# Kernel optimization log

Hardware: AMD Instinct MI355X
Metric: run time of the kernel (lower is better)

The kernel has to match this reference:

```python
import jax, jax.numpy as jnp
import numpy as np
import math

# Model dims
B, S, D, H = 2, 2048, 1024, 16
DH = D // H  # 64
TAU = 0.2
EPS = 1e-5

# Unit-scaling scale factors (constraint = gmean of fwd/bwd scales)
# Linear: gmean(fan_in**-0.5, fan_out**-0.5) = (fan_in*fan_out)**-0.25
# Matmul (m,k)@(k,n): gmean(k**-0.5, n**-0.5, m**-0.5) = (m*k*n)**(-1/6)
# Softmax over dim n: gmean(n/1.31, n/1.65) (empirical constants from unit_scaling)
# GELU: gmean(1/0.588, 1/0.675)
MM_SCALE = (S * S * DH) ** (-1.0 / 6.0)
SM_SCALE = S / math.sqrt(1.31 * 1.65)
GELU_SCALE = (0.588 * 0.675) ** -0.5
SQRT_TAU = math.sqrt(TAU)
SQRT_1MTAU = math.sqrt(1.0 - TAU)


def u_linear(x, w, b=None):
    fan_out, fan_in = w.shape
    scale = (fan_in * fan_out) ** -0.25
    y = x @ w.T
    if b is not None:
        y = y + b
    return y * scale


def layer_norm(x, w, b):
    m = jnp.mean(x, axis=-1, keepdims=True)
    v = jnp.mean(jnp.square(x - m), axis=-1, keepdims=True)
    return (x - m) * jax.lax.rsqrt(v + EPS) * w + b


def setup_inputs() -> dict:
    key = jax.random.key(0)
    ks = jax.random.split(key, 8)
    return {
        "x": jax.random.normal(ks[0], (B, S, D), jnp.float32),
        "w_qkv": jax.random.normal(ks[1], (3 * D, D), jnp.float32),
        "w_o": jax.random.normal(ks[2], (D, D), jnp.float32),
        "w1": jax.random.normal(ks[3], (4 * D, D), jnp.float32),
        "b1": jnp.zeros((4 * D,), jnp.float32),
        "w2": jax.random.normal(ks[4], (D, 4 * D), jnp.float32),
        "b2": jnp.zeros((D,), jnp.float32),
        "ln1_w": jnp.ones((D,), jnp.float32),
        "ln1_b": jnp.zeros((D,), jnp.float32),
        "ln2_w": jnp.ones((D,), jnp.float32),
        "ln2_b": jnp.zeros((D,), jnp.float32),
    }


def reference(x, w_qkv, w_o, w1, b1, w2, b2, ln1_w, ln1_b, ln2_w, ln2_b):
    # --- MHSA branch (residual_split forward is identity; tau enters at add) ---
    skip = x
    h = layer_norm(x, ln1_w, ln1_b)
    qkv = u_linear(h, w_qkv)  # [B,S,3D]
    # einops 'b s (d z h) -> z b h s d' with z=3, h=H
    qkv = qkv.reshape(B, S, DH, 3, H)
    q = jnp.transpose(qkv[:, :, :, 0, :], (0, 3, 1, 2))  # [B,H,S,DH]
    k = jnp.transpose(qkv[:, :, :, 1, :], (0, 3, 1, 2))
    v = jnp.transpose(qkv[:, :, :, 2, :], (0, 3, 1, 2))
    scores = jnp.einsum("bhsd,bhtd->bhst", q, k) * MM_SCALE
    attn = jax.nn.softmax(scores, axis=-1) * SM_SCALE
    # dropout: eval mode -> identity
    av = jnp.einsum("bhst,bhtd->bhsd", attn, v) * MM_SCALE
    av = jnp.transpose(av, (0, 2, 1, 3)).reshape(B, S, D)  # b h s d -> b s (h d)
    attn_out = u_linear(av, w_o)
    x = SQRT_TAU * attn_out + SQRT_1MTAU * skip  # residual_add

    # --- MLP branch ---
    skip = x
    h = layer_norm(x, ln2_w, ln2_b)
    h = u_linear(h, w1, b1)
    h = jax.nn.gelu(h, approximate=False) * GELU_SCALE
    h = u_linear(h, w2, b2)
    return SQRT_TAU * h + SQRT_1MTAU * skip
```

## Files before the change

kernel.cpp:

```cpp
#include <hip/hip_runtime.h>
#include <hip/hip_bf16.h>
#include <math.h>

typedef __hip_bfloat16 bf16;
typedef __attribute__((ext_vector_type(8))) short short8;
typedef __attribute__((ext_vector_type(4))) float floatx4;

#define B_   2
#define S_   2048
#define D_   1024
#define H_   16
#define DH_  64
#define BS_  4096
#define D3_  3072
#define DF_  4096

__device__ __forceinline__ float tof(float v) { return v; }
__device__ __forceinline__ float tof(bf16 v) { return __bfloat162float(v); }

__device__ __forceinline__ void gload_lds16(const bf16* g, bf16* l) {
  __builtin_amdgcn_global_load_lds(
      (const __attribute__((address_space(1))) unsigned int*)g,
      (__attribute__((address_space(3))) unsigned int*)l, 16, 0, 0);
}

#define VMCNT(n) asm volatile("s_waitcnt vmcnt(" #n ")" ::: "memory")

__global__ __launch_bounds__(256) void cvt_all(
    const float* __restrict__ wqkv, const float* __restrict__ wo,
    const float* __restrict__ w1, bf16* __restrict__ wqb,
    bf16* __restrict__ wob, bf16* __restrict__ w1b) {
  const int g = blockIdx.x * 256 + threadIdx.x;
  if (g < 786432) {
    const int n2 = g >> 8;
    const int col = (g & 255) * 4;
    const int z = n2 >> 10, hh = (n2 >> 6) & 15, d = n2 & 63;
    const int n = d * 48 + z * 16 + hh;
    float4 v = *(const float4*)(wqkv + (size_t)n * 1024 + col);
    bf16 o[4] = {__float2bfloat16(v.x), __float2bfloat16(v.y),
                 __float2bfloat16(v.z), __float2bfloat16(v.w)};
    *(unsigned long long*)(wqb + (size_t)n2 * 1024 + col) =
        *(unsigned long long*)o;
  } else if (g < 1048576) {
    const int g2 = g - 786432;
    float4 v = ((const float4*)wo)[g2];
    bf16 o[4] = {__float2bfloat16(v.x), __float2bfloat16(v.y),
                 __float2bfloat16(v.z), __float2bfloat16(v.w)};
    ((unsigned long long*)wob)[g2] = *(unsigned long long*)o;
  } else {
    const int g2 = g - 1048576;
    float4 v = ((const float4*)w1)[g2];
    bf16 o[4] = {__float2bfloat16(v.x), __float2bfloat16(v.y),
                 __float2bfloat16(v.z), __float2bfloat16(v.w)};
    ((unsigned long long*)w1b)[g2] = *(unsigned long long*)o;
  }
}

template <bool FUSE, bool INIT, typename TA, typename TS>
__global__ __launch_bounds__(256) void resid_ln_kernel(
    const TA* __restrict__ a, const TA* __restrict__ a2,
    const TS* __restrict__ skip,
    const float* __restrict__ w, const float* __restrict__ bias,
    bf16* __restrict__ hout, float st, float s1t,
    float* __restrict__ oinit, const float* __restrict__ b2,
    float cb, float cs) {
  const int row = blockIdx.x;
  const int tid = threadIdx.x;
  const int base = tid * 4;
  const size_t roff = (size_t)row * D_;

  float xv[4];
#pragma unroll
  for (int i = 0; i < 4; i++) {
    float v = tof(a[roff + base + i]);
    if (FUSE) v = st * (v + tof(a2[roff + base + i]))
                  + s1t * tof(skip[roff + base + i]);
    xv[i] = v;
  }
  if (INIT) {
#pragma unroll
    for (int i = 0; i < 4; i++)
      oinit[roff + base + i] = cs * xv[i] + cb * b2[base + i];
  }

  float ls = 0.f, lq = 0.f;
#pragma unroll
  for (int i = 0; i < 4; i++) { ls += xv[i]; lq += xv[i] * xv[i]; }

  __shared__ float ssum[256];
  __shared__ float ssq[256];
  ssum[tid] = ls; ssq[tid] = lq;
  __syncthreads();
  for (int off = 128; off > 0; off >>= 1) {
    if (tid < off) { ssum[tid] += ssum[tid + off]; ssq[tid] += ssq[tid + off]; }
    __syncthreads();
  }
  const float mean = ssum[0] * (1.0f / D_);
  const float var  = ssq[0] * (1.0f / D_) - mean * mean;
  const float rstd = rsqrtf(var + 1e-5f);

#pragma unroll
  for (int i = 0; i < 4; i++) {
    float v = (xv[i] - mean) * rstd * w[base + i] + bias[base + i];
    hout[roff + base + i] = __float2bfloat16(v);
  }
}

__global__ __launch_bounds__(256) void reduce_ffn2(
    const bf16* __restrict__ p0, const bf16* __restrict__ p1,
    float* __restrict__ out, float sc) {
  const size_t i = ((size_t)blockIdx.x * 256 + threadIdx.x) * 8;
  short8 a = *(const short8*)(p0 + i);
  short8 b = *(const short8*)(p1 + i);
  bf16 t0[8], t1[8];
  *(short8*)t0 = a; *(short8*)t1 = b;
  float4 o0 = *(float4*)(out + i);
  float4 o1 = *(float4*)(out + i + 4);
#pragma unroll
  for (int e = 0; e < 4; e++) {
    ((float*)&o0)[e] += sc * (__bfloat162float(t0[e]) + __bfloat162float(t1[e]));
    ((float*)&o1)[e] += sc * (__bfloat162float(t0[e + 4]) + __bfloat162float(t1[e + 4]));
  }
  *(float4*)(out + i) = o0;
  *(float4*)(out + i + 4) = o1;
}

__global__ __launch_bounds__(256) void combine_attn(
    const bf16* __restrict__ O0, const bf16* __restrict__ O1,
    const float* __restrict__ l0, const float* __restrict__ l1,
    bf16* __restrict__ att, float sc) {
  const size_t i = ((size_t)blockIdx.x * 256 + threadIdx.x) * 8;
  const int srow = (int)(i >> 10);
  const int h = (int)(i >> 6) & 15;
  const float inv = sc / (l0[srow * H_ + h] + l1[srow * H_ + h]);
  short8 a = *(const short8*)(O0 + i);
  short8 b = *(const short8*)(O1 + i);
  bf16 t0[8], t1[8], o[8];
  *(short8*)t0 = a; *(short8*)t1 = b;
#pragma unroll
  for (int e = 0; e < 8; e++)
    o[e] = __float2bfloat16((tof(t0[e]) + tof(t1[e])) * inv);
  *(short8*)(att + i) = *(short8*)o;
}

template <int EPI, bool FCVT, typename TC>
__global__ __launch_bounds__(512, 2) void gemm_mfma256(
    const bf16* __restrict__ A, const bf16* __restrict__ Bw,
    TC* __restrict__ C, TC* __restrict__ Chi,
    int M, int N, int K, float scale,
    const float* __restrict__ bias, float st,
    const float* __restrict__ cvsrc, bf16* __restrict__ cvdst, int cvn4) {
  const int nbx = N >> 8;
  const int nwg = nbx * (M >> 8);
  if (FCVT && (int)blockIdx.x >= nwg) {
    const int nth = ((int)gridDim.x - nwg) * 512;
    for (int i = ((int)blockIdx.x - nwg) * 512 + (int)threadIdx.x; i < cvn4;
         i += nth) {
      float4 v = ((const float4*)cvsrc)[i];
      bf16 o[4] = {__float2bfloat16(v.x), __float2bfloat16(v.y),
                   __float2bfloat16(v.z), __float2bfloat16(v.w)};
      ((unsigned long long*)cvdst)[i] = *(unsigned long long*)o;
    }
    return;
  }

  __shared__ __align__(16) bf16 As[2][2][128][64];
  __shared__ __align__(16) bf16 Bs[2][2][128][64];

  const int tid = threadIdx.x;
  const int lane = tid & 63;
  const int w = tid >> 6;
  const int wm = w >> 2;
  const int wn = w & 3;
  const int quad = lane >> 4;
  const int l16 = lane & 15;

  int bid = blockIdx.x;
  bid = (bid & 7) * (nwg >> 3) + (bid >> 3);
  const size_t bm = (size_t)(bid / nbx) * 256;
  const size_t bn = (size_t)(bid % nbx) * 256;

  const bf16* gsrc[4][2];
  bf16* ldsp[4][2];
#pragma unroll
  for (int i = 0; i < 2; i++) {
    const int G = tid + i * 512;
    const int cr = G >> 3;
    const int gs8 = ((G & 7) ^ (cr & 7)) * 8;
    const int ra = ((cr >> 6) << 7) + (cr & 63);
    const int rb = ((cr >> 5) << 6) + (cr & 31);
    gsrc[0][i] = A  + (bm + ra) * (size_t)K + gs8;
    gsrc[2][i] = A  + (bm + ra + 64) * (size_t)K + gs8;
    gsrc[1][i] = Bw + (bn + rb) * (size_t)K + gs8;
    gsrc[3][i] = Bw + (bn + rb + 32) * (size_t)K + gs8;
    ldsp[0][i] = &As[0][0][0][0] + G * 8;
    ldsp[2][i] = &As[0][1][0][0] + G * 8;
    ldsp[1][i] = &Bs[0][0][0][0] + G * 8;
    ldsp[3][i] = &Bs[0][1][0][0] + G * 8;
  }

  auto STAGE = [&](int c, int tn) {
    const int boff = (tn & 1) * 16384;
    gload_lds16(gsrc[c][0] + (size_t)tn * 64, ldsp[c][0] + boff);
    gload_lds16(gsrc[c][1] + (size_t)tn * 64, ldsp[c][1] + boff);
  };

  const int ksw0 = (quad ^ (l16 & 7)) * 8;
  const int ksw1 = ((4 + quad) ^ (l16 & 7)) * 8;

  floatx4 acc[8][4];
#pragma unroll
  for (int i = 0; i < 8; i++)
#pragma unroll
    for (int j = 0; j < 4; j++) acc[i][j] = {0.f, 0.f, 0.f, 0.f};

  short8 af[4][2], bv[2][2];

  auto READ_A = [&](int b, int h) {
#pragma unroll
    for (int mf = 0; mf < 4; mf++) {
      const bf16* p = &As[b][h][wm * 64 + mf * 16 + l16][0];
      af[mf][0] = *(const short8*)(p + ksw0);
      af[mf][1] = *(const short8*)(p + ksw1);
    }
  };
  auto READ_B = [&](int b, int bh) {
#pragma unroll
    for (int nf = 0; nf < 2; nf++) {
      const bf16* p = &Bs[b][bh][wn * 32 + nf * 16 + l16][0];
      bv[nf][0] = *(const short8*)(p + ksw0);
      bv[nf][1] = *(const short8*)(p + ksw1);
    }
  };
  auto MFMA16 = [&](int mb, int nb) {
#pragma unroll
    for (int mf = 0; mf < 4; mf++)
#pragma unroll
      for (int nf = 0; nf < 2; nf++) {
        floatx4 c = acc[mb + mf][nb + nf];
        c = __builtin_amdgcn_mfma_f32_16x16x32_bf16(af[mf][0], bv[nf][0], c, 0, 0, 0);
        c = __builtin_amdgcn_mfma_f32_16x16x32_bf16(af[mf][1], bv[nf][1], c, 0, 0, 0);
        acc[mb + mf][nb + nf] = c;
      }
  };

  STAGE(0, 0); STAGE(1, 0); STAGE(2, 0); STAGE(3, 0);
  VMCNT(4);
  __builtin_amdgcn_s_barrier();
  __builtin_amdgcn_sched_barrier(0);

  const int NT = K >> 6;
#pragma unroll 1
  for (int t = 0; t < NT; t++) {
    const int b = t & 1;
    const bool nl = (t + 1 < NT);
    READ_A(b, 0);
    READ_B(b, 0);
    if (nl) STAGE(0, t + 1);
    __builtin_amdgcn_s_barrier();
    __builtin_amdgcn_sched_barrier(0);
    __builtin_amdgcn_s_setprio(1);
    MFMA16(0, 0);
    __builtin_amdgcn_s_setprio(0);
    if (nl) { VMCNT(2); } else { VMCNT(0); }
    __builtin_amdgcn_s_barrier();
    __builtin_amdgcn_sched_barrier(0);
    READ_B(b, 1);
    if (nl) STAGE(1, t + 1);
    __builtin_amdgcn_s_barrier();
    __builtin_amdgcn_sched_barrier(0);
    __builtin_amdgcn_s_setprio(1);
    MFMA16(0, 2);
    __builtin_amdgcn_s_setprio(0);
    __builtin_amdgcn_s_barrier();
    __builtin_amdgcn_sched_barrier(0);
    READ_A(b, 1);
    if (nl) STAGE(2, t + 1);
    __builtin_amdgcn_s_barrier();
    __builtin_amdgcn_sched_barrier(0);
    __builtin_amdgcn_s_setprio(1);
    MFMA16(4, 2);
    __builtin_amdgcn_s_setprio(0);
    __builtin_amdgcn_s_barrier();
    __builtin_amdgcn_sched_barrier(0);
    READ_B(b, 0);
    if (nl) STAGE(3, t + 1);
    __builtin_amdgcn_s_barrier();
    __builtin_amdgcn_sched_barrier(0);
    __builtin_amdgcn_s_setprio(1);
    MFMA16(4, 0);
    __builtin_amdgcn_s_setprio(0);
    if (nl) { VMCNT(4); } else { VMCNT(0); }
    __builtin_amdgcn_s_barrier();
    __builtin_amdgcn_sched_barrier(0);
  }

  TC* Cb = (bm < 1024) ? C : Chi;
  const size_t rsub = (bm < 1024) ? 0 : 1024;
  float sc_eff = scale;
  if (EPI == 2) sc_eff = (bn < 1024) ? st : scale;
  float bias4[4];
  if (EPI == 1) {
#pragma unroll
    for (int j = 0; j < 4; j++) bias4[j] = bias[bn + wn * 64 + j * 16 + l16];
  }
#pragma unroll
  for (int mi = 0; mi < 8; mi++) {
    const size_t r0 =
        bm - rsub + wm * 128 + (mi >> 2) * 64 + (mi & 3) * 16 + quad * 4;
#pragma unroll
    for (int r = 0; r < 4; r++) {
      const size_t rowoff = (r0 + r) * (size_t)N + bn + wn * 64 + l16;
#pragma unroll
      for (int j = 0; j < 4; j++) {
        float v = acc[mi][j][r];
        if (EPI == 2) {
          Cb[rowoff + j * 16] = __float2bfloat16(v * sc_eff);
        } else {
          float u = (v + bias4[j]) * scale;
          float tt = u * (0.7978845608f + 0.0356774081f * u * u);
          float e = __builtin_amdgcn_exp2f(tt * 2.8853900818f);
          float th = 1.0f - 2.0f * __builtin_amdgcn_rcpf(e + 1.0f);
          Cb[rowoff + j * 16] =
              __float2bfloat16(0.5f * u * (1.0f + th) * st);
        }
      }
    }
  }
}

__global__ __launch_bounds__(512, 2) void gemm_mfma128(
    const bf16* __restrict__ A, const bf16* __restrict__ Ahi,
    const bf16* __restrict__ Bw,
    bf16* __restrict__ C, bf16* __restrict__ C2, int M, int N, int K) {
  __shared__ __align__(16) bf16 As[2][2][128][64];
  __shared__ __align__(16) bf16 Bs[2][2][64][64];

  const int tid = threadIdx.x;
  const int lane = tid & 63;
  const int w = tid >> 6;
  const int wm = w >> 2;
  const int wn = w & 3;
  const int quad = lane >> 4;
  const int l16 = lane & 15;

  const int nbx = N >> 7;
  const int nwg = nbx * (M >> 8) * 2;
  int bid = blockIdx.x;
  bid = (bid & 7) * (nwg >> 3) + (bid >> 3);
  const int split = bid & 1;
  const int tile = bid >> 1;
  const size_t bm = (size_t)(tile / nbx) * 256;
  const size_t bn = (size_t)(tile % nbx) * 128;
  const int lda = K * 2;
  const int koff = split * K;

  const bf16* Ab = (bm < 1024) ? A : Ahi;
  const size_t bmr = (bm < 1024) ? bm : bm - 1024;

  const bf16* gA[2][2];
  bf16* lA[2][2];
#pragma unroll
  for (int i = 0; i < 2; i++) {
    const int G = tid + i * 512;
    const int cr = G >> 3;
    const int gs8 = ((G & 7) ^ (cr & 7)) * 8;
    const int ra = ((cr >> 6) << 7) + (cr & 63);
    gA[0][i] = Ab + (bmr + ra) * (size_t)lda + koff + gs8;
    gA[1][i] = Ab + (bmr + ra + 64) * (size_t)lda + koff + gs8;
    lA[0][i] = &As[0][0][0][0] + G * 8;
    lA[1][i] = &As[0][1][0][0] + G * 8;
  }
  const bf16* gB[2];
  bf16* lB[2];
  {
    const int cr = tid >> 3;
    const int gs8 = ((tid & 7) ^ (cr & 7)) * 8;
    gB[0] = Bw + (bn + cr) * (size_t)lda + koff + gs8;
    gB[1] = Bw + (bn + 64 + cr) * (size_t)lda + koff + gs8;
    lB[0] = &Bs[0][0][0][0] + tid * 8;
    lB[1] = &Bs[0][1][0][0] + tid * 8;
  }

  auto STAGE_A = [&](int h, int tn) {
    const int boff = (tn & 1) * 16384;
    gload_lds16(gA[h][0] + (size_t)tn * 64, lA[h][0] + boff);
    gload_lds16(gA[h][1] + (size_t)tn * 64, lA[h][1] + boff);
  };
  auto STAGE_B = [&](int bh, int tn) {
    const int boff = (tn & 1) * 8192;
    gload_lds16(gB[bh] + (size_t)tn * 64, lB[bh] + boff);
  };

  const int ksw0 = (quad ^ (l16 & 7)) * 8;
  const int ksw1 = ((4 + quad) ^ (l16 & 7)) * 8;

  floatx4 acc[8][2];
#pragma unroll
  for (int i = 0; i < 8; i++)
#pragma unroll
    for (int j = 0; j < 2; j++) acc[i][j] = {0.f, 0.f, 0.f, 0.f};

  short8 af[4][2], bv[2][2];

  auto READ_A = [&](int b, int h) {
#pragma unroll
    for (int mf = 0; mf < 4; mf++) {
      const bf16* p = &As[b][h][wm * 64 + mf * 16 + l16][0];
      af[mf][0] = *(const short8*)(p + ksw0);
      af[mf][1] = *(const short8*)(p + ksw1);
    }
  };
  auto READ_BNF = [&](int b, int nf) {
    const bf16* p = &Bs[b][wn >> 1][(wn & 1) * 32 + nf * 16 + l16][0];
    bv[nf][0] = *(const short8*)(p + ksw0);
    bv[nf][1] = *(const short8*)(p + ksw1);
  };
  auto MFMA8 = [&](int mb, int nf) {
#pragma unroll
    for (int mf = 0; mf < 4; mf++) {
      floatx4 c = acc[mb + mf][nf];
      c = __builtin_amdgcn_mfma_f32_16x16x32_bf16(af[mf][0], bv[nf][0], c, 0, 0, 0);
      c = __builtin_amdgcn_mfma_f32_16x16x32_bf16(af[mf][1], bv[nf][1], c, 0, 0, 0);
      acc[mb + mf][nf] = c;
    }
  };

  STAGE_A(0, 0); STAGE_B(0, 0); STAGE_B(1, 0); STAGE_A(1, 0);
  VMCNT(2);
  __builtin_amdgcn_s_barrier();
  __builtin_amdgcn_sched_barrier(0);

  const int NT = K >> 6;
#pragma unroll 1
  for (int t = 0; t < NT; t++) {
    const int b = t & 1;
    const bool nl = (t + 1 < NT);
    READ_A(b, 0);
    READ_BNF(b, 0);
    if (nl) STAGE_A(0, t + 1);
    __builtin_amdgcn_s_barrier();
    __builtin_amdgcn_sched_barrier(0);
    __builtin_amdgcn_s_setprio(1);
    MFMA8(0, 0);
    __builtin_amdgcn_s_setprio(0);
    __builtin_amdgcn_s_barrier();
    __builtin_amdgcn_sched_barrier(0);
    READ_BNF(b, 1);
    if (nl) STAGE_B(0, t + 1);
    __builtin_amdgcn_s_barrier();
    __builtin_amdgcn_sched_barrier(0);
    __builtin_amdgcn_s_setprio(1);
    MFMA8(0, 1);
    __builtin_amdgcn_s_setprio(0);
    if (nl) { VMCNT(3); } else { VMCNT(0); }
    __builtin_amdgcn_s_barrier();
    __builtin_amdgcn_sched_barrier(0);
    READ_A(b, 1);
    if (nl) STAGE_B(1, t + 1);
    __builtin_amdgcn_s_barrier();
    __builtin_amdgcn_sched_barrier(0);
    __builtin_amdgcn_s_setprio(1);
    MFMA8(4, 1);
    __builtin_amdgcn_s_setprio(0);
    __builtin_amdgcn_s_barrier();
    __builtin_amdgcn_sched_barrier(0);
    if (nl) STAGE_A(1, t + 1);
    __builtin_amdgcn_s_barrier();
    __builtin_amdgcn_sched_barrier(0);
    __builtin_amdgcn_s_setprio(1);
    MFMA8(4, 0);
    __builtin_amdgcn_s_setprio(0);
    if (nl) { VMCNT(2); } else { VMCNT(0); }
    __builtin_amdgcn_s_barrier();
    __builtin_amdgcn_sched_barrier(0);
  }

  bf16* dst = split ? C2 : C;
#pragma unroll
  for (int mi = 0; mi < 8; mi++) {
    const size_t r0 = bm + wm * 128 + (mi >> 2) * 64 + (mi & 3) * 16 + quad * 4;
#pragma unroll
    for (int r = 0; r < 4; r++) {
      const size_t rowoff = (r0 + r) * (size_t)N + bn + wn * 32 + l16;
#pragma unroll
      for (int j = 0; j < 2; j++)
        dst[rowoff + j * 16] = __float2bfloat16(acc[mi][j][r]);
    }
  }
}

__global__ __launch_bounds__(512) void flash_attn_mfma(
    const bf16* __restrict__ qkv, bf16* __restrict__ O0,
    bf16* __restrict__ O1, float* __restrict__ lb0,
    float* __restrict__ lb1) {
  const int flat = (blockIdx.z * H_ + blockIdx.y) * 32 + blockIdx.x;
  const int g8 = flat & 7, slot = flat >> 3;
  const int hf = g8 * 4 + (slot >> 5);
  const int rem = slot & 31;
  const int qb = (rem >> 1) * 128;
  const int half = rem & 1;
  const int h = hf & 15, b = hf >> 4;

  const int tid = threadIdx.x;
  const int lane = tid & 63;
  const int wv = tid >> 6;
  const int quad = lane >> 4;
  const int l16 = lane & 15;

  __shared__ __align__(16) bf16 Ks[2][64][64];
  __shared__ __align__(16) bf16 Vt[2][64][64];
  __shared__ __align__(16) bf16 Ps[128][64];

  const bf16* Qb_ = qkv + (size_t)b * S_ * D3_ + h * DH_;
  const bf16* Kb_ = Qb_ + 1024 + (size_t)half * 1024 * D3_;
  const bf16* Vb_ = Qb_ + 2048 + (size_t)half * 1024 * D3_;

  short8 bq0, bq1;
  {
    const bf16* qrow = Qb_ + (size_t)(qb + wv * 16 + l16) * D3_ + quad * 8;
    bq0 = *(const short8*)(qrow);
    bq1 = *(const short8*)(qrow + 32);
  }

  float l_part = 0.f;
  floatx4 o[4];
#pragma unroll
  for (int fd = 0; fd < 4; fd++) o[fd] = {0.f, 0.f, 0.f, 0.f};

  const int prow = wv * 16 + l16;
  const int psw = (prow & 7) << 4;
  char* pbase = (char*)&Ps[0][0] + prow * 128;

  const bf16* ksrc =
      Kb_ + (size_t)(tid >> 3) * D3_ + (((tid & 7) ^ ((tid >> 3) & 7)) * 8);
  bf16* kdst = &Ks[0][0][0] + tid * 8;
  const int vj = tid & 63, vd = (tid >> 6) * 8;
  const int vjg = vj >> 3, vjr = vj & 7;

  const int ksw0 = (quad ^ (l16 & 7)) * 8;
  const int ksw1 = ((4 + quad) ^ (l16 & 7)) * 8;

  gload_lds16(ksrc, kdst);
  uint4 vreg = *(const uint4*)(Vb_ + (size_t)vj * D3_ + vd);

  const int NT = 1024 / 64;
#pragma unroll 1
  for (int t = 0; t < NT; t++) {
    const int cur = t & 1;
    {
      bf16 tmp[8];
      *(uint4*)tmp = vreg;
#pragma unroll
      for (int e = 0; e < 8; e++)
        Vt[cur][vd + e][((vjg ^ e) << 3) | vjr] = tmp[e];
    }
    __syncthreads();

    if (t + 1 < NT) {
      gload_lds16(ksrc + (size_t)(t + 1) * 64 * D3_, kdst + (cur ^ 1) * 4096);
      vreg = *(const uint4*)(Vb_ + (size_t)((t + 1) * 64 + vj) * D3_ + vd);
    }

    float st[4][4];
    __builtin_amdgcn_s_setprio(1);
#pragma unroll
    for (int fk = 0; fk < 4; fk++) {
      const bf16* kp = &Ks[cur][fk * 16 + l16][0];
      short8 ak0 = *(const short8*)(kp + ksw0);
      short8 ak1 = *(const short8*)(kp + ksw1);
      floatx4 acc = {0.f, 0.f, 0.f, 0.f};
      acc = __builtin_amdgcn_mfma_f32_16x16x32_bf16(ak0, bq0, acc, 0, 0, 0);
      acc = __builtin_amdgcn_mfma_f32_16x16x32_bf16(ak1, bq1, acc, 0, 0, 0);
#pragma unroll
      for (int r = 0; r < 4; r++) st[fk][r] = acc[r];
    }
    __builtin_amdgcn_s_setprio(0);

#pragma unroll
    for (int fk = 0; fk < 2; fk++) {
      bf16 pk[4];
#pragma unroll
      for (int r = 0; r < 4; r++) {
        const float p = __builtin_amdgcn_exp2f(st[fk][r]);
        l_part += p;
        pk[r] = __float2bfloat16(p);
      }
      *(uint2*)(pbase + ((fk * 32 + quad * 8) ^ psw)) = *(uint2*)pk;
    }
    short8 ap0 = *(const short8*)(pbase + ((quad * 16) ^ psw));
#pragma unroll
    for (int fk = 2; fk < 4; fk++) {
      bf16 pk[4];
#pragma unroll
      for (int r = 0; r < 4; r++) {
        const float p = __builtin_amdgcn_exp2f(st[fk][r]);
        l_part += p;
        pk[r] = __float2bfloat16(p);
      }
      *(uint2*)(pbase + ((fk * 32 + quad * 8) ^ psw)) = *(uint2*)pk;
    }
    short8 ap1 = *(const short8*)(pbase + ((64 + quad * 16) ^ psw));

    __builtin_amdgcn_s_setprio(1);
#pragma unroll
    for (int fd = 0; fd < 4; fd++) {
      const bf16* vp = &Vt[cur][fd * 16 + l16][0];
      short8 bv0 = *(const short8*)(vp + ksw0);
      short8 bv1 = *(const short8*)(vp + ksw1);
      o[fd] = __builtin_amdgcn_mfma_f32_16x16x32_bf16(ap0, bv0, o[fd], 0, 0, 0);
      o[fd] = __builtin_amdgcn_mfma_f32_16x16x32_bf16(ap1, bv1, o[fd], 0, 0, 0);
    }
    __builtin_amdgcn_s_setprio(0);
  }

  l_part += __shfl_xor(l_part, 16);
  l_part += __shfl_xor(l_part, 32);

  bf16* Oo = half ? O1 : O0;
  float* lo = half ? lb1 : lb0;
  if (quad == 0)
    lo[(size_t)(b * S_ + qb + wv * 16 + l16) * H_ + h] = l_part;
#pragma unroll
  for (int r = 0; r < 4; r++) {
    const size_t base =
        ((size_t)(b * S_ + qb + wv * 16 + quad * 4 + r)) * D_ + h * DH_;
#pragma unroll
    for (int fd = 0; fd < 4; fd++)
      Oo[base + fd * 16 + l16] = __float2bfloat16(o[fd][r]);
  }
}

extern "C" void kernel_launch(void* const* d_in, const int* in_sizes, int n_in,
                              void* d_out, int out_size, void* d_ws, size_t ws_size,
                              hipStream_t stream) {
  const float* x     = (const float*)d_in[0];
  const float* w_qkv = (const float*)d_in[1];
  const float* w_o   = (const float*)d_in[2];
  const float* w1    = (const float*)d_in[3];
  const float* b1    = (const float*)d_in[4];
  const float* w2    = (const float*)d_in[5];
  const float* b2    = (const float*)d_in[6];
  const float* ln1w  = (const float*)d_in[7];
  const float* ln1b  = (const float*)d_in[8];
  const float* ln2w  = (const float*)d_in[9];
  const float* ln2b  = (const float*)d_in[10];
  float* out = (float*)d_out;
  bf16* ws  = (bf16*)d_ws;

  bf16* h1   = ws;
  bf16* wqb  = ws + 4194304;
  bf16* wob  = ws + 7340032;
  bf16* qkv  = ws + 8388608;
  bf16* w2b  = ws + 20971520;
  bf16* w1b  = ws + 25165824;
  bf16* Ob0  = (bf16*)out;
  bf16* Ob1  = (bf16*)out + 4194304;
  float* l0f = (float*)(ws + 4194304);
  float* l1f = l0f + 65536;
  bf16* att  = ws;
  bf16* Po   = ws + 8388608;
  bf16* h2   = ws + 4194304;
  bf16* gl   = ws;
  bf16* gh   = ws + 8388608;
  bf16* Pf0  = ws + 4194304;
  bf16* Pf1  = ws + 25165824;

  const float MM_SCALE   = (float)pow((double)S_ * S_ * DH_, -1.0 / 6.0);
  const float SM_SCALE   = (float)((double)S_ / sqrt(1.31 * 1.65));
  const float GELU_SCALE = (float)pow(0.588 * 0.675, -0.5);
  const float SQRT_TAU   = (float)sqrt(0.2);
  const float SQRT_1MT   = (float)sqrt(0.8);
  const float LOG2E      = 1.4426950408889634f;
  const float qkv_scale  = (float)pow((double)D_ * D3_, -0.25);
  const float o_scale    = (float)pow((double)D_ * D_, -0.25);
  const float w1_scale   = (float)pow((double)D_ * DF_, -0.25);
  const float w2_scale   = (float)pow((double)DF_ * D_, -0.25);

  cvt_all<<<8192, 256, 0, stream>>>(w_qkv, w_o, w1, wqb, wob, w1b);
  resid_ln_kernel<false, false, float, float><<<BS_, 256, 0, stream>>>(
      x, nullptr, nullptr, ln1w, ln1b, h1, 0.f, 0.f, nullptr, nullptr, 0.f, 0.f);
  gemm_mfma256<2, true, bf16><<<dim3(256), 512, 0, stream>>>(
      h1, wqb, qkv, qkv + (size_t)1024 * D3_, BS_, D3_, D_, qkv_scale,
      nullptr, qkv_scale * MM_SCALE * LOG2E, w2, w2b, D_ * DF_ / 4);
  flash_attn_mfma<<<dim3(32, H_, B_), 512, 0, stream>>>(
      qkv, Ob0, Ob1, l0f, l1f);
  combine_attn<<<2048, 256, 0, stream>>>(
      Ob0, Ob1, l0f, l1f, att, SM_SCALE * MM_SCALE);
  gemm_mfma128<<<dim3(256), 512, 0, stream>>>(
      att, att + (size_t)1024 * D_, wob, Po, Po + (size_t)BS_ * D_,
      BS_, D_, D_ / 2);
  resid_ln_kernel<true, true, bf16, float><<<BS_, 256, 0, stream>>>(
      Po, Po + (size_t)BS_ * D_, x, ln2w, ln2b, h2,
      SQRT_TAU * o_scale, SQRT_1MT, out, b2, SQRT_TAU * w2_scale, SQRT_1MT);
  gemm_mfma256<1, false, bf16><<<dim3(256), 512, 0, stream>>>(
      h2, w1b, gl, gh, BS_, DF_, D_, w1_scale, b1, GELU_SCALE,
      nullptr, nullptr, 0);
  gemm_mfma128<<<dim3(256), 512, 0, stream>>>(
      gl, gh, w2b, Pf0, Pf1, BS_, D_, DF_ / 2);
  reduce_ffn2<<<2048, 256, 0, stream>>>(Pf0, Pf1, out, SQRT_TAU * w2_scale);
}
```

Measured before the change: 332.3 us.

## Double query rows per attention block and fuse LN1 into weight convert

The flash attention kernel now processes two 128-row query groups per block, so each loaded K/V tile is reused for 256 queries and the grid is halved. The first layer norm is folded into the weight conversion kernel as extra blocks, removing a separate launch. This trades higher register and LDS use per block, and fewer blocks in flight, for less K/V load traffic. The fused layer norm computes variance in one pass as E[x^2]-mean^2.

```diff
diff --git a/kernel.cpp b/kernel.cpp
--- a/kernel.cpp
+++ b/kernel.cpp
@@ -29,8 +29,40 @@
 __global__ __launch_bounds__(256) void cvt_all(
     const float* __restrict__ wqkv, const float* __restrict__ wo,
     const float* __restrict__ w1, bf16* __restrict__ wqb,
-    bf16* __restrict__ wob, bf16* __restrict__ w1b) {
-  const int g = blockIdx.x * 256 + threadIdx.x;
+    bf16* __restrict__ wob, bf16* __restrict__ w1b,
+    const float* __restrict__ x, const float* __restrict__ ln1w,
+    const float* __restrict__ ln1b, bf16* __restrict__ h1) {
+  __shared__ float ssum[256];
+  __shared__ float ssq[256];
+  const int bid = blockIdx.x;
+  const int tid = threadIdx.x;
+  if (bid >= 8192) {
+    const int row = bid - 8192;
+    const int base = tid * 4;
+    const size_t roff = (size_t)row * D_;
+    float xv[4];
+#pragma unroll
+    for (int i = 0; i < 4; i++) xv[i] = x[roff + base + i];
+    float ls = 0.f, lq = 0.f;
+#pragma unroll
+    for (int i = 0; i < 4; i++) { ls += xv[i]; lq += xv[i] * xv[i]; }
+    ssum[tid] = ls; ssq[tid] = lq;
+    __syncthreads();
+    for (int off = 128; off > 0; off >>= 1) {
+      if (tid < off) { ssum[tid] += ssum[tid + off]; ssq[tid] += ssq[tid + off]; }
+      __syncthreads();
+    }
+    const float mean = ssum[0] * (1.0f / D_);
+    const float var  = ssq[0] * (1.0f / D_) - mean * mean;
+    const float rstd = rsqrtf(var + 1e-5f);
+#pragma unroll
+    for (int i = 0; i < 4; i++) {
+      float v = (xv[i] - mean) * rstd * ln1w[base + i] + ln1b[base + i];
+      h1[roff + base + i] = __float2bfloat16(v);
+    }
+    return;
+  }
+  const int g = bid * 256 + tid;
   if (g < 786432) {
     const int n2 = g >> 8;
     const int col = (g & 255) * 4;
@@ -494,11 +526,11 @@
     const bf16* __restrict__ qkv, bf16* __restrict__ O0,
     bf16* __restrict__ O1, float* __restrict__ lb0,
     float* __restrict__ lb1) {
-  const int flat = (blockIdx.z * H_ + blockIdx.y) * 32 + blockIdx.x;
+  const int flat = (blockIdx.z * H_ + blockIdx.y) * 16 + blockIdx.x;
   const int g8 = flat & 7, slot = flat >> 3;
-  const int hf = g8 * 4 + (slot >> 5);
-  const int rem = slot & 31;
-  const int qb = (rem >> 1) * 128;
+  const int hf = g8 * 4 + (slot >> 4);
+  const int rem = slot & 15;
+  const int qb = (rem >> 1) * 256;
   const int half = rem & 1;
   const int h = hf & 15, b = hf >> 4;
 
@@ -510,27 +542,33 @@
 
   __shared__ __align__(16) bf16 Ks[2][64][64];
   __shared__ __align__(16) bf16 Vt[2][64][64];
-  __shared__ __align__(16) bf16 Ps[128][64];
+  __shared__ __align__(16) bf16 Ps[256][64];
 
   const bf16* Qb_ = qkv + (size_t)b * S_ * D3_ + h * DH_;
   const bf16* Kb_ = Qb_ + 1024 + (size_t)half * 1024 * D3_;
   const bf16* Vb_ = Qb_ + 2048 + (size_t)half * 1024 * D3_;
 
-  short8 bq0, bq1;
-  {
-    const bf16* qrow = Qb_ + (size_t)(qb + wv * 16 + l16) * D3_ + quad * 8;
-    bq0 = *(const short8*)(qrow);
-    bq1 = *(const short8*)(qrow + 32);
-  }
-
-  float l_part = 0.f;
-  floatx4 o[4];
-#pragma unroll
-  for (int fd = 0; fd < 4; fd++) o[fd] = {0.f, 0.f, 0.f, 0.f};
+  short8 bq[2][2];
+#pragma unroll
+  for (int qg = 0; qg < 2; qg++) {
+    const bf16* qrow =
+        Qb_ + (size_t)(qb + qg * 128 + wv * 16 + l16) * D3_ + quad * 8;
+    bq[qg][0] = *(const short8*)(qrow);
+    bq[qg][1] = *(const short8*)(qrow + 32);
+  }
+
+  float l_part[2] = {0.f, 0.f};
+  floatx4 o[2][4];
+#pragma unroll
+  for (int qg = 0; qg < 2; qg++)
+#pragma unroll
+    for (int fd = 0; fd < 4; fd++) o[qg][fd] = {0.f, 0.f, 0.f, 0.f};
 
   const int prow = wv * 16 + l16;
   const int psw = (prow & 7) << 4;
-  char* pbase = (char*)&Ps[0][0] + prow * 128;
+  char* pb[2];
+  pb[0] = (char*)&Ps[0][0] + prow * 128;
+  pb[1] = pb[0] + 128 * 128;
 
   const bf16* ksrc =
       Kb_ + (size_t)(tid >> 3) * D3_ + (((tid & 7) ^ ((tid >> 3) & 7)) * 8);
@@ -562,45 +600,44 @@
       vreg = *(const uint4*)(Vb_ + (size_t)((t + 1) * 64 + vj) * D3_ + vd);
     }
 
-    float st[4][4];
+    float st[2][4][4];
     __builtin_amdgcn_s_setprio(1);
 #pragma unroll
     for (int fk = 0; fk < 4; fk++) {
       const bf16* kp = &Ks[cur][fk * 16 + l16][0];
       short8 ak0 = *(const short8*)(kp + ksw0);
       short8 ak1 = *(const short8*)(kp + ksw1);
-      floatx4 acc = {0.f, 0.f, 0.f, 0.f};
-      acc = __builtin_amdgcn_mfma_f32_16x16x32_bf16(ak0, bq0, acc, 0, 0, 0);
-      acc = __builtin_amdgcn_mfma_f32_16x16x32_bf16(ak1, bq1, acc, 0, 0, 0);
-#pragma unroll
-      for (int r = 0; r < 4; r++) st[fk][r] = acc[r];
-    }
-    __builtin_amdgcn_s_setprio(0);
-
-#pragma unroll
-    for (int fk = 0; fk < 2; fk++) {
-      bf16 pk[4];
-#pragma unroll
-      for (int r = 0; r < 4; r++) {
-        const float p = __builtin_amdgcn_exp2f(st[fk][r]);
-        l_part += p;
-        pk[r] = __float2bfloat16(p);
+#pragma unroll
+      for (int qg = 0; qg < 2; qg++) {
+        floatx4 acc = {0.f, 0.f, 0.f, 0.f};
+        acc = __builtin_amdgcn_mfma_f32_16x16x32_bf16(ak0, bq[qg][0], acc, 0, 0, 0);
+        acc = __builtin_amdgcn_mfma_f32_16x16x32_bf16(ak1, bq[qg][1], acc, 0, 0, 0);
+#pragma unroll
+        for (int r = 0; r < 4; r++) st[qg][fk][r] = acc[r];
       }
-      *(uint2*)(pbase + ((fk * 32 + quad * 8) ^ psw)) = *(uint2*)pk;
-    }
-    short8 ap0 = *(const short8*)(pbase + ((quad * 16) ^ psw));
-#pragma unroll
-    for (int fk = 2; fk < 4; fk++) {
-      bf16 pk[4];
-#pragma unroll
-      for (int r = 0; r < 4; r++) {
-        const float p = __builtin_amdgcn_exp2f(st[fk][r]);
-        l_part += p;
-        pk[r] = __float2bfloat16(p);
+    }
+    __builtin_amdgcn_s_setprio(0);
+
+#pragma unroll
+    for (int qg = 0; qg < 2; qg++)
+#pragma unroll
+      for (int fk = 0; fk < 4; fk++) {
+        bf16 pk[4];
+#pragma unroll
+        for (int r = 0; r < 4; r++) {
+          const float p = __builtin_amdgcn_exp2f(st[qg][fk][r]);
+          l_part[qg] += p;
+          pk[r] = __float2bfloat16(p);
+        }
+        *(uint2*)(pb[qg] + ((fk * 32 + quad * 8) ^ psw)) = *(uint2*)pk;
       }
-      *(uint2*)(pbase + ((fk * 32 + quad * 8) ^ psw)) = *(uint2*)pk;
-    }
-    short8 ap1 = *(const short8*)(pbase + ((64 + quad * 16) ^ psw));
+
+    short8 ap[2][2];
+#pragma unroll
+    for (int qg = 0; qg < 2; qg++) {
+      ap[qg][0] = *(const short8*)(pb[qg] + ((quad * 16) ^ psw));
+      ap[qg][1] = *(const short8*)(pb[qg] + ((64 + quad * 16) ^ psw));
+    }
 
     __builtin_amdgcn_s_setprio(1);
 #pragma unroll
@@ -608,26 +645,33 @@
       const bf16* vp = &Vt[cur][fd * 16 + l16][0];
       short8 bv0 = *(const short8*)(vp + ksw0);
       short8 bv1 = *(const short8*)(vp + ksw1);
-      o[fd] = __builtin_amdgcn_mfma_f32_16x16x32_bf16(ap0, bv0, o[fd], 0, 0, 0);
-      o[fd] = __builtin_amdgcn_mfma_f32_16x16x32_bf16(ap1, bv1, o[fd], 0, 0, 0);
-    }
-    __builtin_amdgcn_s_setprio(0);
-  }
-
-  l_part += __shfl_xor(l_part, 16);
-  l_part += __shfl_xor(l_part, 32);
+#pragma unroll
+      for (int qg = 0; qg < 2; qg++) {
+        o[qg][fd] = __builtin_amdgcn_mfma_f32_16x16x32_bf16(ap[qg][0], bv0, o[qg][fd], 0, 0, 0);
+        o[qg][fd] = __builtin_amdgcn_mfma_f32_16x16x32_bf16(ap[qg][1], bv1, o[qg][fd], 0, 0, 0);
+      }
+    }
+    __builtin_amdgcn_s_setprio(0);
+  }
 
   bf16* Oo = half ? O1 : O0;
   float* lo = half ? lb1 : lb0;
-  if (quad == 0)
-    lo[(size_t)(b * S_ + qb + wv * 16 + l16) * H_ + h] = l_part;
-#pragma unroll
-  for (int r = 0; r < 4; r++) {
-    const size_t base =
-        ((size_t)(b * S_ + qb + wv * 16 + quad * 4 + r)) * D_ + h * DH_;
-#pragma unroll
-    for (int fd = 0; fd < 4; fd++)
-      Oo[base + fd * 16 + l16] = __float2bfloat16(o[fd][r]);
+#pragma unroll
+  for (int qg = 0; qg < 2; qg++) {
+    float lp = l_part[qg];
+    lp += __shfl_xor(lp, 16);
+    lp += __shfl_xor(lp, 32);
+    if (quad == 0)
+      lo[(size_t)(b * S_ + qb + qg * 128 + wv * 16 + l16) * H_ + h] = lp;
+#pragma unroll
+    for (int r = 0; r < 4; r++) {
+      const size_t base =
+          ((size_t)(b * S_ + qb + qg * 128 + wv * 16 + quad * 4 + r)) * D_ +
+          h * DH_;
+#pragma unroll
+      for (int fd = 0; fd < 4; fd++)
+        Oo[base + fd * 16 + l16] = __float2bfloat16(o[qg][fd][r]);
+    }
   }
 }
 
@@ -677,13 +721,12 @@
   const float w1_scale   = (float)pow((double)D_ * DF_, -0.25);
   const float w2_scale   = (float)pow((double)DF_ * D_, -0.25);
 
-  cvt_all<<<8192, 256, 0, stream>>>(w_qkv, w_o, w1, wqb, wob, w1b);
-  resid_ln_kernel<false, false, float, float><<<BS_, 256, 0, stream>>>(
-      x, nullptr, nullptr, ln1w, ln1b, h1, 0.f, 0.f, nullptr, nullptr, 0.f, 0.f);
+  cvt_all<<<12288, 256, 0, stream>>>(w_qkv, w_o, w1, wqb, wob, w1b,
+                                     x, ln1w, ln1b, h1);
   gemm_mfma256<2, true, bf16><<<dim3(256), 512, 0, stream>>>(
       h1, wqb, qkv, qkv + (size_t)1024 * D3_, BS_, D3_, D_, qkv_scale,
       nullptr, qkv_scale * MM_SCALE * LOG2E, w2, w2b, D_ * DF_ / 4);
-  flash_attn_mfma<<<dim3(32, H_, B_), 512, 0, stream>>>(
+  flash_attn_mfma<<<dim3(16, H_, B_), 512, 0, stream>>>(
       qkv, Ob0, Ob1, l0f, l1f);
   combine_attn<<<2048, 256, 0, stream>>>(
       Ob0, Ob1, l0f, l1f, att, SM_SCALE * MM_SCALE);
```

Measured after the change: 341.7 us. 1.03x slower.
